# Performance work log

Hardware: AMD Instinct MI355X
Metric: run time of the kernel (lower is better)

The kernel has to match this reference:

```python
import jax, jax.numpy as jnp
import numpy as np

B, D_IN, D_OUT = 8192, 1024, 1024


def setup_inputs() -> dict:
    key = jax.random.key(0)
    k1, k2 = jax.random.split(key)
    x = jax.random.normal(k1, (B, D_IN), dtype=jnp.float32)
    # Keras add_weight(shape=(3, input_dim, output_dim), initializer='uniform')
    kernel = jax.random.normal(k2, (3, D_IN, D_OUT), dtype=jnp.float32) * 0.05
    return {"x": x, "kernel": kernel}


def reference(x, kernel):
    # x: (B, D). Layer does expand_dims(axis=1) -> (B, 1, D) (seq_len == 1).
    output_dim = kernel.shape[-1]
    xe = x[:, None, :]                                   # (B, 1, D)
    q = jnp.einsum('bsd,do->bso', xe, kernel[0])         # (B, 1, O)
    k = jnp.einsum('bsd,do->bso', xe, kernel[1])         # (B, 1, O)
    v = jnp.einsum('bsd,do->bso', xe, kernel[2])         # (B, 1, O)
    scores = jnp.einsum('bqo,bko->bqk', q, k) / jnp.sqrt(
        jnp.asarray(output_dim, x.dtype))                # (B, 1, 1)
    attn = jax.nn.softmax(scores, axis=-1)
    out = jnp.einsum('bqk,bko->bqo', attn, v)            # (B, 1, O)
    return out
```

## Files before the change

kernel.cpp:

```cpp
#include <hip/hip_runtime.h>
#include <hip/hip_bf16.h>
#include <stdint.h>

#define AS1 __attribute__((address_space(1)))
#define AS3 __attribute__((address_space(3)))

typedef __attribute__((ext_vector_type(8))) short bf16x8_t;
typedef __attribute__((ext_vector_type(4))) float f32x4_t;

#define DDIM 1024
#define WT_ELEMS ((size_t)DDIM * DDIM)
#define XB_ELEMS ((size_t)8192 * DDIM)

static __device__ inline ushort f32_to_bf16_rne(float f) {
  union { float f; uint32_t u; } v;
  v.f = f;
  v.u += 0x7FFFu + ((v.u >> 16) & 1u);
  return (ushort)(v.u >> 16);
}

__global__ __launch_bounds__(256) void prep(const float* __restrict__ W,
                                            ushort* __restrict__ Wt,
                                            const float* __restrict__ X,
                                            ushort* __restrict__ Xb) {
  if (blockIdx.x < 256) {
    __shared__ float tile[64][65];
    const int t  = threadIdx.x;
    const int bk = blockIdx.x & 15;
    const int bn = blockIdx.x >> 4;
#pragma unroll
    for (int s = 0; s < 4; ++s) {
      const int slot = (s << 8) + t;
      const int r    = slot >> 4;
      const int c4   = (slot & 15) << 2;
      const float4 v = *(const float4*)(W + (size_t)(bk * 64 + r) * DDIM + bn * 64 + c4);
      tile[r][c4 + 0] = v.x; tile[r][c4 + 1] = v.y;
      tile[r][c4 + 2] = v.z; tile[r][c4 + 3] = v.w;
    }
    __syncthreads();
#pragma unroll
    for (int s = 0; s < 2; ++s) {
      const int slot = (s << 8) + t;
      const int n    = slot >> 3;
      const int k8   = (slot & 7) << 3;
      union { ushort h[8]; uint4 u; } tmp;
#pragma unroll
      for (int j = 0; j < 8; ++j) tmp.h[j] = f32_to_bf16_rne(tile[k8 + j][n]);
      *(uint4*)(Wt + (size_t)(bn * 64 + n) * DDIM + bk * 64 + k8) = tmp.u;
    }
  } else {
    const size_t i = ((size_t)(blockIdx.x - 256) * 256 + threadIdx.x) << 3;
    const float4 v0 = *(const float4*)(X + i);
    const float4 v1 = *(const float4*)(X + i + 4);
    union { ushort h[8]; uint4 u; } o;
    o.h[0] = f32_to_bf16_rne(v0.x); o.h[1] = f32_to_bf16_rne(v0.y);
    o.h[2] = f32_to_bf16_rne(v0.z); o.h[3] = f32_to_bf16_rne(v0.w);
    o.h[4] = f32_to_bf16_rne(v1.x); o.h[5] = f32_to_bf16_rne(v1.y);
    o.h[6] = f32_to_bf16_rne(v1.z); o.h[7] = f32_to_bf16_rne(v1.w);
    *(uint4*)(Xb + i) = o.u;
  }
}

__global__ __launch_bounds__(256, 2) void gemm_bb(const ushort* __restrict__ Xb,
                                                  const ushort* __restrict__ Wt,
                                                  float* __restrict__ C) {
  __shared__ __align__(16) ushort As[2][128 * 64];
  __shared__ __align__(16) ushort Bs[2][128 * 64];

  const int t    = threadIdx.x;
  const int wave = t >> 6;
  const int lane = t & 63;
  const int m0 = blockIdx.x * 128;
  const int n0 = blockIdx.y * 128;

  const int sr = t >> 3;
  const int sc = (t & 7) ^ (sr & 7);
  const ushort* aB = Xb + (size_t)(m0 + sr) * DDIM + (sc << 3);
  const ushort* bB = Wt + (size_t)(n0 + sr) * DDIM + (sc << 3);

  AS3 char* lA = (AS3 char*)&As[0][0];
  AS3 char* lB = (AS3 char*)&Bs[0][0];
  const int woff = wave << 10;

  const int wr = (wave >> 1) << 6;
  const int wc = (wave & 1) << 6;
  const int fr = lane & 15;
  const int fq = lane >> 4;

  f32x4_t acc[4][4] = {};

  auto issue = [&](int kt, int p) {
    const ushort* a = aB + kt;
    const ushort* b = bB + kt;
    AS3 char* dA = lA + (p << 14) + woff;
    AS3 char* dB = lB + (p << 14) + woff;
#pragma unroll
    for (int j = 0; j < 4; ++j) {
      __builtin_amdgcn_global_load_lds((const AS1 void*)(a + (size_t)(j << 5) * DDIM),
                                       (AS3 void*)(dA + (j << 12)), 16, 0, 0);
      __builtin_amdgcn_global_load_lds((const AS1 void*)(b + (size_t)(j << 5) * DDIM),
                                       (AS3 void*)(dB + (j << 12)), 16, 0, 0);
    }
  };

  issue(0, 0);

  for (int i = 0; i < 16; ++i) {
    const int p = i & 1;
    if (i < 15) {
      issue((i + 1) << 6, p ^ 1);
      asm volatile("s_waitcnt vmcnt(8)\n\ts_barrier" ::: "memory");
    } else {
      asm volatile("s_waitcnt vmcnt(0)\n\ts_barrier" ::: "memory");
    }

    const ushort* Ab = &As[p][0];
    const ushort* Bb = &Bs[p][0];
#pragma unroll
    for (int ks = 0; ks < 2; ++ks) {
      const int kc = (ks << 2) + fq;
      bf16x8_t af[4], bfr[4];
#pragma unroll
      for (int mi = 0; mi < 4; ++mi) {
        const int r = wr + (mi << 4) + fr;
        af[mi] = *(const bf16x8_t*)&Ab[(r << 6) + ((kc ^ (r & 7)) << 3)];
      }
#pragma unroll
      for (int ni = 0; ni < 4; ++ni) {
        const int r = wc + (ni << 4) + fr;
        bfr[ni] = *(const bf16x8_t*)&Bb[(r << 6) + ((kc ^ (r & 7)) << 3)];
      }
#pragma unroll
      for (int mi = 0; mi < 4; ++mi)
#pragma unroll
        for (int ni = 0; ni < 4; ++ni)
          acc[mi][ni] = __builtin_amdgcn_mfma_f32_16x16x32_bf16(af[mi], bfr[ni], acc[mi][ni], 0, 0, 0);
    }
    asm volatile("s_barrier" ::: "memory");
  }

#pragma unroll
  for (int mi = 0; mi < 4; ++mi) {
#pragma unroll
    for (int r = 0; r < 4; ++r) {
      const int row = m0 + wr + (mi << 4) + (fq << 2) + r;
      float* crow = C + (size_t)row * DDIM + n0 + wc + fr;
#pragma unroll
      for (int ni = 0; ni < 4; ++ni)
        crow[ni << 4] = acc[mi][ni][r];
    }
  }
}

__global__ __launch_bounds__(256) void gemm_xw(const float* __restrict__ X,
                                               const ushort* __restrict__ Wt,
                                               float* __restrict__ C) {
  __shared__ __align__(16) ushort As[128 * 32];
  __shared__ __align__(16) ushort Bs[128 * 32];
  const int t    = threadIdx.x;
  const int wave = t >> 6;
  const int lane = t & 63;
  const int m0 = blockIdx.x * 128;
  const int n0 = blockIdx.y * 128;
  const int srow  = (wave << 4) + (lane >> 2);
  const int skcol = (lane & 3) << 3;
  const ushort* bptr0 = Wt + (size_t)(n0 + srow) * DDIM + skcol;
  const ushort* bptr1 = Wt + (size_t)(n0 + 64 + srow) * DDIM + skcol;
  const int ar = t >> 2;
  const int ak = (t & 3) << 3;
  const float* aptr0 = X + (size_t)(m0 + ar) * DDIM + ak;
  const float* aptr1 = X + (size_t)(m0 + 64 + ar) * DDIM + ak;
  ushort* asw0 = &As[(ar << 5) + ak];
  ushort* asw1 = &As[((ar + 64) << 5) + ak];
  const int wr = (wave >> 1) << 6;
  const int wc = (wave & 1) << 6;
  const int fr = lane & 15;
  const int fq = lane >> 4;
  f32x4_t acc[4][4] = {};
  AS3 char* ldsB = (AS3 char*)Bs;
  const int woff = wave << 10;
  for (int kt = 0; kt < DDIM; kt += 32) {
    const float4 a00 = *(const float4*)(aptr0);
    const float4 a01 = *(const float4*)(aptr0 + 4);
    const float4 a10 = *(const float4*)(aptr1);
    const float4 a11 = *(const float4*)(aptr1 + 4);
    aptr0 += 32; aptr1 += 32;
    __syncthreads();
    __builtin_amdgcn_global_load_lds((const AS1 void*)bptr0, (AS3 void*)(ldsB + woff),        16, 0, 0);
    __builtin_amdgcn_global_load_lds((const AS1 void*)bptr1, (AS3 void*)(ldsB + 4096 + woff), 16, 0, 0);
    bptr0 += 32; bptr1 += 32;
    union { ushort h[8]; bf16x8_t v; } c0, c1;
    c0.h[0] = f32_to_bf16_rne(a00.x); c0.h[1] = f32_to_bf16_rne(a00.y);
    c0.h[2] = f32_to_bf16_rne(a00.z); c0.h[3] = f32_to_bf16_rne(a00.w);
    c0.h[4] = f32_to_bf16_rne(a01.x); c0.h[5] = f32_to_bf16_rne(a01.y);
    c0.h[6] = f32_to_bf16_rne(a01.z); c0.h[7] = f32_to_bf16_rne(a01.w);
    c1.h[0] = f32_to_bf16_rne(a10.x); c1.h[1] = f32_to_bf16_rne(a10.y);
    c1.h[2] = f32_to_bf16_rne(a10.z); c1.h[3] = f32_to_bf16_rne(a10.w);
    c1.h[4] = f32_to_bf16_rne(a11.x); c1.h[5] = f32_to_bf16_rne(a11.y);
    c1.h[6] = f32_to_bf16_rne(a11.z); c1.h[7] = f32_to_bf16_rne(a11.w);
    *(bf16x8_t*)asw0 = c0.v;
    *(bf16x8_t*)asw1 = c1.v;
    __syncthreads();
    bf16x8_t af[4], bfr[4];
#pragma unroll
    for (int mi = 0; mi < 4; ++mi)
      af[mi] = *(const bf16x8_t*)&As[((wr + (mi << 4) + fr) << 5) + (fq << 3)];
#pragma unroll
    for (int ni = 0; ni < 4; ++ni)
      bfr[ni] = *(const bf16x8_t*)&Bs[((wc + (ni << 4) + fr) << 5) + (fq << 3)];
#pragma unroll
    for (int mi = 0; mi < 4; ++mi)
#pragma unroll
      for (int ni = 0; ni < 4; ++ni)
        acc[mi][ni] = __builtin_amdgcn_mfma_f32_16x16x32_bf16(af[mi], bfr[ni], acc[mi][ni], 0, 0, 0);
  }
#pragma unroll
  for (int mi = 0; mi < 4; ++mi)
#pragma unroll
    for (int r = 0; r < 4; ++r) {
      const int row = m0 + wr + (mi << 4) + (fq << 2) + r;
      float* crow = C + (size_t)row * DDIM + n0 + wc + fr;
#pragma unroll
      for (int ni = 0; ni < 4; ++ni)
        crow[ni << 4] = acc[mi][ni][r];
    }
}

extern "C" void kernel_launch(void* const* d_in, const int* in_sizes, int n_in,
                              void* d_out, int out_size, void* d_ws, size_t ws_size,
                              hipStream_t stream) {
  const float* x    = (const float*)d_in[0];
  const float* kern = (const float*)d_in[1];
  const float* W = kern + (size_t)2 * DDIM * DDIM;
  ushort* Wt = (ushort*)d_ws;
  const int M = in_sizes[0] / DDIM;

  if (ws_size >= (WT_ELEMS + XB_ELEMS) * sizeof(ushort)) {
    ushort* Xb = (ushort*)d_ws + WT_ELEMS;
    const unsigned cvt_blocks = (unsigned)((size_t)M * DDIM / 8 / 256);
    prep<<<256 + cvt_blocks, 256, 0, stream>>>(W, Wt, x, Xb);
    gemm_bb<<<dim3(M / 128, DDIM / 128), 256, 0, stream>>>(Xb, Wt, (float*)d_out);
  } else {
    prep<<<256, 256, 0, stream>>>(W, Wt, x, (ushort*)nullptr);
    gemm_xw<<<dim3(M / 128, DDIM / 128), 256, 0, stream>>>(x, Wt, (float*)d_out);
  }
}
```

Measured before the change: 112.0 us.

## Deepen bf16 GEMM LDS pipeline to four stages with 32-wide K tiles

The bf16 GEMM's LDS staging changes from two buffers of 64-wide K tiles to four buffers of 32-wide K tiles. Three tiles of global-to-LDS loads stay in flight while one tile is computed, with a new XOR swizzle matched to the 64-byte rows. The aim is to hide global-load latency better at the same total LDS footprint. In exchange there are twice as many barrier-separated iterations, fewer MFMAs per barrier, and a hand-written epilogue that drains the last three stages.

```diff
diff --git a/kernel.cpp b/kernel.cpp
--- a/kernel.cpp
+++ b/kernel.cpp
@@ -64,8 +64,8 @@
 __global__ __launch_bounds__(256, 2) void gemm_bb(const ushort* __restrict__ Xb,
                                                   const ushort* __restrict__ Wt,
                                                   float* __restrict__ C) {
-  __shared__ __align__(16) ushort As[2][128 * 64];
-  __shared__ __align__(16) ushort Bs[2][128 * 64];
+  __shared__ __align__(16) ushort As[4][128 * 32];
+  __shared__ __align__(16) ushort Bs[4][128 * 32];
 
   const int t    = threadIdx.x;
   const int wave = t >> 6;
@@ -73,8 +73,8 @@
   const int m0 = blockIdx.x * 128;
   const int n0 = blockIdx.y * 128;
 
-  const int sr = t >> 3;
-  const int sc = (t & 7) ^ (sr & 7);
+  const int sr = t >> 2;
+  const int sc = (t & 3) ^ ((sr >> 1) & 3);
   const ushort* aB = Xb + (size_t)(m0 + sr) * DDIM + (sc << 3);
   const ushort* bB = Wt + (size_t)(n0 + sr) * DDIM + (sc << 3);
 
@@ -89,55 +89,59 @@
 
   f32x4_t acc[4][4] = {};
 
-  auto issue = [&](int kt, int p) {
-    const ushort* a = aB + kt;
-    const ushort* b = bB + kt;
-    AS3 char* dA = lA + (p << 14) + woff;
-    AS3 char* dB = lB + (p << 14) + woff;
-#pragma unroll
-    for (int j = 0; j < 4; ++j) {
-      __builtin_amdgcn_global_load_lds((const AS1 void*)(a + (size_t)(j << 5) * DDIM),
+  auto issue = [&](int st) {
+    const int p = st & 3;
+    const ushort* a = aB + (st << 5);
+    const ushort* b = bB + (st << 5);
+    AS3 char* dA = lA + (p << 13) + woff;
+    AS3 char* dB = lB + (p << 13) + woff;
+#pragma unroll
+    for (int j = 0; j < 2; ++j) {
+      __builtin_amdgcn_global_load_lds((const AS1 void*)(a + (size_t)(j << 6) * DDIM),
                                        (AS3 void*)(dA + (j << 12)), 16, 0, 0);
-      __builtin_amdgcn_global_load_lds((const AS1 void*)(b + (size_t)(j << 5) * DDIM),
+      __builtin_amdgcn_global_load_lds((const AS1 void*)(b + (size_t)(j << 6) * DDIM),
                                        (AS3 void*)(dB + (j << 12)), 16, 0, 0);
     }
   };
 
-  issue(0, 0);
-
-  for (int i = 0; i < 16; ++i) {
-    const int p = i & 1;
-    if (i < 15) {
-      issue((i + 1) << 6, p ^ 1);
-      asm volatile("s_waitcnt vmcnt(8)\n\ts_barrier" ::: "memory");
-    } else {
-      asm volatile("s_waitcnt vmcnt(0)\n\ts_barrier" ::: "memory");
-    }
-
+  auto compute = [&](int p) {
     const ushort* Ab = &As[p][0];
     const ushort* Bb = &Bs[p][0];
-#pragma unroll
-    for (int ks = 0; ks < 2; ++ks) {
-      const int kc = (ks << 2) + fq;
-      bf16x8_t af[4], bfr[4];
-#pragma unroll
-      for (int mi = 0; mi < 4; ++mi) {
-        const int r = wr + (mi << 4) + fr;
-        af[mi] = *(const bf16x8_t*)&Ab[(r << 6) + ((kc ^ (r & 7)) << 3)];
-      }
-#pragma unroll
-      for (int ni = 0; ni < 4; ++ni) {
-        const int r = wc + (ni << 4) + fr;
-        bfr[ni] = *(const bf16x8_t*)&Bb[(r << 6) + ((kc ^ (r & 7)) << 3)];
-      }
-#pragma unroll
-      for (int mi = 0; mi < 4; ++mi)
-#pragma unroll
-        for (int ni = 0; ni < 4; ++ni)
-          acc[mi][ni] = __builtin_amdgcn_mfma_f32_16x16x32_bf16(af[mi], bfr[ni], acc[mi][ni], 0, 0, 0);
-    }
+    bf16x8_t af[4], bfr[4];
+#pragma unroll
+    for (int mi = 0; mi < 4; ++mi) {
+      const int r = wr + (mi << 4) + fr;
+      af[mi] = *(const bf16x8_t*)&Ab[(r << 5) + ((fq ^ ((r >> 1) & 3)) << 3)];
+    }
+#pragma unroll
+    for (int ni = 0; ni < 4; ++ni) {
+      const int r = wc + (ni << 4) + fr;
+      bfr[ni] = *(const bf16x8_t*)&Bb[(r << 5) + ((fq ^ ((r >> 1) & 3)) << 3)];
+    }
+#pragma unroll
+    for (int mi = 0; mi < 4; ++mi)
+#pragma unroll
+      for (int ni = 0; ni < 4; ++ni)
+        acc[mi][ni] = __builtin_amdgcn_mfma_f32_16x16x32_bf16(af[mi], bfr[ni], acc[mi][ni], 0, 0, 0);
+  };
+
+  issue(0);
+  issue(1);
+  issue(2);
+  asm volatile("s_waitcnt vmcnt(8)\n\ts_barrier" ::: "memory");
+
+  for (int i = 0; i < 29; ++i) {
+    issue(i + 3);
+    asm volatile("s_waitcnt vmcnt(12)\n\ts_barrier" ::: "memory");
+    compute(i & 3);
     asm volatile("s_barrier" ::: "memory");
   }
+  asm volatile("s_waitcnt vmcnt(8)\n\ts_barrier" ::: "memory");
+  compute(1);
+  asm volatile("s_waitcnt vmcnt(4)\n\ts_barrier" ::: "memory");
+  compute(2);
+  asm volatile("s_waitcnt vmcnt(0)\n\ts_barrier" ::: "memory");
+  compute(3);
 
 #pragma unroll
   for (int mi = 0; mi < 4; ++mi) {
```

New measurement: 115.4 us. 1.03x slower.
